# Kernel optimization log

Measured on AMD Instinct MI355X. Metric: run time of the kernel, lower is better.

The kernel has to match this reference:

```python
import jax, jax.numpy as jnp
import numpy as np

J = 24  # fixed pooling window (SampleLength/N = 1200/50)


def setup_inputs() -> dict:
    key = jax.random.key(0)
    k1, k2, k3 = jax.random.split(key, 3)
    T, N, K, C = 786432, 50, 400, 10  # T = 32768 segments * J
    x = jax.random.normal(k1, (T, N), dtype=jnp.float32)
    W1 = jax.random.normal(k2, (K, N), dtype=jnp.float32) * 0.1
    W2 = jax.random.normal(k3, (C, K), dtype=jnp.float32) * 0.1
    return {"x": x, "W1": W1, "W2": W2}


def reference(x, W1, W2):
    # linear + relu: [T, N] @ [N, K] -> [T, K]
    local_features = jax.nn.relu(jnp.einsum('tn,kn->tk', x, W1))
    # fixed-window mean over consecutive J rows: [T, K] -> [T//J, K]
    T, K = local_features.shape
    features = local_features.reshape(T // J, J, K).mean(axis=1)
    # final linear: [T//J, K] @ [K, C] -> [T//J, C]
    logits = jnp.einsum('bk,ck->bc', features, W2)
    return logits
```

## Files before the change

### kernel.cpp

```cpp
#include <hip/hip_runtime.h>
#include <hip/hip_bf16.h>

#define T_TOTAL 786432
#define N_IN 50
#define K_FEAT 400
#define C_OUT 10
#define ROWS_PER_CHUNK 48
#define NCHUNKS (T_TOTAL / ROWS_PER_CHUNK)
#define CPB 4
#define NBLOCKS (NCHUNKS / CPB)
#define NTHREADS 320
#define XS_STRIDE 72
#define XS_ROWS (CPB * ROWS_PER_CHUNK)

#define W1F_TASKS (25 * 2 * 64)
#define W2T_OFF_BYTES 51200
#define W2T_FLOATS (25 * NTHREADS)
#define PREP_TASKS (W1F_TASKS + W2T_FLOATS)

typedef __bf16 bfx8 __attribute__((ext_vector_type(8)));
typedef short  s16x8 __attribute__((ext_vector_type(8)));
typedef float  f32x4 __attribute__((ext_vector_type(4)));

static __device__ __forceinline__ short f2bf(float f) {
    union { float f; unsigned u; } v; v.f = f;
    unsigned r = v.u + 0x7fffu + ((v.u >> 16) & 1u);
    return (short)(r >> 16);
}

__global__ void prep_kernel(const float* __restrict__ W1,
                            const float* __restrict__ W2,
                            short* __restrict__ w1f, float* __restrict__ w2t)
{
    const int gid = blockIdx.x * blockDim.x + threadIdx.x;
    if (gid < W1F_TASKS) {
        const int lane = gid & 63;
        const int s    = (gid >> 6) & 1;
        const int tile = gid >> 7;
        const int m16  = lane & 15;
        const int quad = lane >> 4;
        const float* row = W1 + (tile * 16 + m16) * N_IN;
        s16x8 v;
        #pragma unroll
        for (int j = 0; j < 8; ++j) {
            const int n = s * 32 + quad * 8 + j;
            v[j] = (n < N_IN) ? f2bf(row[n]) : (short)0;
        }
        *(s16x8*)&w1f[gid * 8] = v;
    } else if (gid < PREP_TASKS) {
        const int i   = gid - W1F_TASKS;
        const int j   = i / NTHREADS;
        const int tid = i - j * NTHREADS;
        const int o    = tid >> 4;
        const int part = tid & 15;
        const int seg  = (o >= 10) ? 1 : 0;
        const int cls  = o - seg * 10;
        w2t[i] = W2[cls * K_FEAT + part * 25 + j];
    }
}

__global__ __launch_bounds__(NTHREADS) void classifier_kernel(
    const float* __restrict__ x, const short* __restrict__ w1f,
    const float* __restrict__ w2t, float* __restrict__ out)
{
    __shared__ short xs[XS_ROWS * XS_STRIDE];
    __shared__ float pooled[2 * K_FEAT];

    const int tid  = threadIdx.x;
    const int wave = tid >> 6;
    const int lane = tid & 63;
    const int m16  = lane & 15;
    const int quad = lane >> 4;

    {
        const float* xb = x + (size_t)blockIdx.x * (XS_ROWS * N_IN);
        #pragma unroll
        for (int it = 0; it < (XS_ROWS * 25) / NTHREADS; ++it) {
            const int i = tid + it * NTHREADS;
            const int r = i / 25;
            const int c2 = i - r * 25;
            const float2 v = *(const float2*)(xb + 2 * i);
            const int packed = (unsigned short)f2bf(v.x) |
                               ((unsigned)(unsigned short)f2bf(v.y) << 16);
            *(int*)&xs[r * XS_STRIDE + 2 * c2] = packed;
        }
        for (int i = tid; i < XS_ROWS * 7; i += NTHREADS) {
            const int r = i / 7;
            const int c = 50 + 2 * (i - r * 7);
            *(int*)&xs[r * XS_STRIDE + c] = 0;
        }
    }

    s16x8 bfrag[5][2];
    {
        const s16x8* wf = (const s16x8*)w1f;
        #pragma unroll
        for (int t = 0; t < 5; ++t) {
            #pragma unroll
            for (int s = 0; s < 2; ++s)
                bfrag[t][s] = wf[((wave * 5 + t) * 2 + s) * 64 + lane];
        }
    }

    const int o    = tid >> 4;
    const int part = tid & 15;
    const int segO = (o >= 10) ? 1 : 0;
    const int cls  = o - segO * 10;
    float w2r[25];
    #pragma unroll
    for (int j = 0; j < 25; ++j) w2r[j] = w2t[j * NTHREADS + tid];

    __syncthreads();

    for (int ciq = 0; ciq < CPB; ++ciq) {
        s16x8 a[3][2];
        #pragma unroll
        for (int r = 0; r < 3; ++r) {
            const short* arow =
                &xs[(ciq * ROWS_PER_CHUNK + r * 16 + m16) * XS_STRIDE + quad * 8];
            a[r][0] = *(const s16x8*)(arow);
            a[r][1] = *(const s16x8*)(arow + 32);
        }

        #pragma unroll
        for (int t = 0; t < 5; ++t) {
            float c0 = 0.f, c1 = 0.f;
            #pragma unroll
            for (int r = 0; r < 3; ++r) {
                f32x4 acc = {0.f, 0.f, 0.f, 0.f};
                acc = __builtin_amdgcn_mfma_f32_16x16x32_bf16(
                        __builtin_bit_cast(bfx8, a[r][0]),
                        __builtin_bit_cast(bfx8, bfrag[t][0]), acc, 0, 0, 0);
                acc = __builtin_amdgcn_mfma_f32_16x16x32_bf16(
                        __builtin_bit_cast(bfx8, a[r][1]),
                        __builtin_bit_cast(bfx8, bfrag[t][1]), acc, 0, 0, 0);
                const float s = fmaxf(acc[0], 0.f) + fmaxf(acc[1], 0.f)
                              + fmaxf(acc[2], 0.f) + fmaxf(acc[3], 0.f);
                const int g = r * 4 + quad;
                if (g < 6) c0 += s; else c1 += s;
            }
            c0 += __shfl_xor(c0, 16);
            c0 += __shfl_xor(c0, 32);
            c1 += __shfl_xor(c1, 16);
            c1 += __shfl_xor(c1, 32);
            if (quad == 0) {
                const int feat = (wave * 5 + t) * 16 + m16;
                pooled[feat] = c0;
                pooled[K_FEAT + feat] = c1;
            }
        }
        __syncthreads();

        float sum = 0.f;
        const float* pv = &pooled[segO * K_FEAT + part * 25];
        #pragma unroll
        for (int j = 0; j < 25; ++j) sum += pv[j] * w2r[j];
        sum += __shfl_down(sum, 8, 16);
        sum += __shfl_down(sum, 4, 16);
        sum += __shfl_down(sum, 2, 16);
        sum += __shfl_down(sum, 1, 16);
        if (part == 0) {
            const int chunk = blockIdx.x * CPB + ciq;
            out[(chunk * 2 + segO) * C_OUT + cls] = sum * (1.0f / 24.0f);
        }
        __syncthreads();
    }
}

extern "C" void kernel_launch(void* const* d_in, const int* in_sizes, int n_in,
                              void* d_out, int out_size, void* d_ws, size_t ws_size,
                              hipStream_t stream) {
    const float* x  = (const float*)d_in[0];
    const float* W1 = (const float*)d_in[1];
    const float* W2 = (const float*)d_in[2];
    float* out = (float*)d_out;

    short* w1f = (short*)d_ws;
    float* w2t = (float*)((char*)d_ws + W2T_OFF_BYTES);

    prep_kernel<<<(PREP_TASKS + 255) / 256, 256, 0, stream>>>(W1, W2, w1f, w2t);
    classifier_kernel<<<NBLOCKS, NTHREADS, 0, stream>>>(x, w1f, w2t, out);
}
```

Before: 288.0 us.

## Split into register-resident phase1 pooling kernel and MFMA phase2 classifier via workspace

Replaces the single LDS-staged kernel with two kernels. Phase 1 has each wave load x rows straight into registers as bf16 MFMA fragments and stream all 25 W1 tiles with a prefetch, writing pooled features as bf16 to a workspace buffer. Phase 2 runs the final 400->10 projection as MFMA over the pooled rows. The aim is to drop the LDS staging and block-level syncs and to raise occupancy. In exchange it adds a global round-trip of pooled features, loses precision by rounding them to bf16, and adds an extra launch. The old kernel is kept as a fallback when the workspace is too small.

```diff
diff --git a/kernel.cpp b/kernel.cpp
--- a/kernel.cpp
+++ b/kernel.cpp
@@ -5,18 +5,17 @@
 #define N_IN 50
 #define K_FEAT 400
 #define C_OUT 10
-#define ROWS_PER_CHUNK 48
-#define NCHUNKS (T_TOTAL / ROWS_PER_CHUNK)
-#define CPB 4
-#define NBLOCKS (NCHUNKS / CPB)
-#define NTHREADS 320
-#define XS_STRIDE 72
-#define XS_ROWS (CPB * ROWS_PER_CHUNK)
+#define NSEG 32768
 
 #define W1F_TASKS (25 * 2 * 64)
 #define W2T_OFF_BYTES 51200
-#define W2T_FLOATS (25 * NTHREADS)
-#define PREP_TASKS (W1F_TASKS + W2T_FLOATS)
+#define W2T_FLOATS (25 * 320)
+#define W2F_OFF_BYTES 83200
+#define W2F_TASKS (13 * 64)
+#define PREP_TASKS (W1F_TASKS + W2T_FLOATS + W2F_TASKS)
+#define POOLED_OFF_BYTES 98304
+#define POOLED_STRIDE 416
+#define WS_NEEDED (POOLED_OFF_BYTES + (size_t)NSEG * POOLED_STRIDE * 2)
 
 typedef __bf16 bfx8 __attribute__((ext_vector_type(8)));
 typedef short  s16x8 __attribute__((ext_vector_type(8)));
@@ -30,7 +29,8 @@
 
 __global__ void prep_kernel(const float* __restrict__ W1,
                             const float* __restrict__ W2,
-                            short* __restrict__ w1f, float* __restrict__ w2t)
+                            short* __restrict__ w1f, float* __restrict__ w2t,
+                            short* __restrict__ w2f)
 {
     const int gid = blockIdx.x * blockDim.x + threadIdx.x;
     if (gid < W1F_TASKS) {
@@ -47,47 +47,181 @@
             v[j] = (n < N_IN) ? f2bf(row[n]) : (short)0;
         }
         *(s16x8*)&w1f[gid * 8] = v;
-    } else if (gid < PREP_TASKS) {
+    } else if (gid < W1F_TASKS + W2T_FLOATS) {
         const int i   = gid - W1F_TASKS;
-        const int j   = i / NTHREADS;
-        const int tid = i - j * NTHREADS;
+        const int j   = i / 320;
+        const int tid = i - j * 320;
         const int o    = tid >> 4;
         const int part = tid & 15;
         const int seg  = (o >= 10) ? 1 : 0;
         const int cls  = o - seg * 10;
         w2t[i] = W2[cls * K_FEAT + part * 25 + j];
-    }
-}
-
-__global__ __launch_bounds__(NTHREADS) void classifier_kernel(
+    } else if (gid < PREP_TASKS) {
+        const int i    = gid - W1F_TASKS - W2T_FLOATS;
+        const int lane = i & 63;
+        const int kt   = i >> 6;
+        const int m16  = lane & 15;
+        const int quad = lane >> 4;
+        s16x8 v;
+        #pragma unroll
+        for (int j = 0; j < 8; ++j) {
+            const int feat = kt * 32 + quad * 8 + j;
+            v[j] = (m16 < C_OUT && feat < K_FEAT) ? f2bf(W2[m16 * K_FEAT + feat])
+                                                  : (short)0;
+        }
+        *(s16x8*)&w2f[i * 8] = v;
+    }
+}
+
+__global__ __launch_bounds__(256, 3) void phase1_kernel(
     const float* __restrict__ x, const short* __restrict__ w1f,
-    const float* __restrict__ w2t, float* __restrict__ out)
+    short* __restrict__ pooled)
 {
-    __shared__ short xs[XS_ROWS * XS_STRIDE];
-    __shared__ float pooled[2 * K_FEAT];
-
     const int tid  = threadIdx.x;
     const int wave = tid >> 6;
     const int lane = tid & 63;
     const int m16  = lane & 15;
     const int quad = lane >> 4;
+    const int wgid = blockIdx.x * 4 + wave;
+    const s16x8* wf = (const s16x8*)w1f;
+
+    for (int g = 0; g < 2; ++g) {
+        const int group = wgid * 2 + g;
+        const float* xg = x + (size_t)group * (2 * 48 * N_IN);
+
+        s16x8 A[6][2];
+        #pragma unroll
+        for (int ct = 0; ct < 6; ++ct) {
+            const float* rp = xg + (ct * 16 + m16) * N_IN;
+            float v0[8], v1[8];
+            #pragma unroll
+            for (int h = 0; h < 4; ++h) {
+                const float2 u = *(const float2*)(rp + quad * 8 + 2 * h);
+                v0[2 * h] = u.x; v0[2 * h + 1] = u.y;
+            }
+            if (quad < 2) {
+                #pragma unroll
+                for (int h = 0; h < 4; ++h) {
+                    const float2 u = *(const float2*)(rp + 32 + quad * 8 + 2 * h);
+                    v1[2 * h] = u.x; v1[2 * h + 1] = u.y;
+                }
+            } else if (quad == 2) {
+                const float2 u = *(const float2*)(rp + 48);
+                v1[0] = u.x; v1[1] = u.y;
+                #pragma unroll
+                for (int j = 2; j < 8; ++j) v1[j] = 0.f;
+            } else {
+                #pragma unroll
+                for (int j = 0; j < 8; ++j) v1[j] = 0.f;
+            }
+            s16x8 f0, f1;
+            #pragma unroll
+            for (int j = 0; j < 8; ++j) { f0[j] = f2bf(v0[j]); f1[j] = f2bf(v1[j]); }
+            A[ct][0] = f0; A[ct][1] = f1;
+        }
+
+        s16x8 b0 = wf[lane];
+        s16x8 b1 = wf[64 + lane];
+        const int seg0 = group * 4;
+        for (int t = 0; t < 25; ++t) {
+            const int tn = (t < 24) ? t + 1 : 24;
+            const s16x8 nb0 = wf[(tn * 2) * 64 + lane];
+            const s16x8 nb1 = wf[(tn * 2 + 1) * 64 + lane];
+            #pragma unroll
+            for (int h = 0; h < 2; ++h) {
+                float c0 = 0.f, c1 = 0.f;
+                #pragma unroll
+                for (int r = 0; r < 3; ++r) {
+                    f32x4 acc = {0.f, 0.f, 0.f, 0.f};
+                    acc = __builtin_amdgcn_mfma_f32_16x16x32_bf16(
+                            __builtin_bit_cast(bfx8, A[h * 3 + r][0]),
+                            __builtin_bit_cast(bfx8, b0), acc, 0, 0, 0);
+                    acc = __builtin_amdgcn_mfma_f32_16x16x32_bf16(
+                            __builtin_bit_cast(bfx8, A[h * 3 + r][1]),
+                            __builtin_bit_cast(bfx8, b1), acc, 0, 0, 0);
+                    const float s = fmaxf(acc[0], 0.f) + fmaxf(acc[1], 0.f)
+                                  + fmaxf(acc[2], 0.f) + fmaxf(acc[3], 0.f);
+                    if (r * 4 + quad < 6) c0 += s; else c1 += s;
+                }
+                c0 += __shfl_xor(c0, 16); c0 += __shfl_xor(c0, 32);
+                c1 += __shfl_xor(c1, 16); c1 += __shfl_xor(c1, 32);
+                if (quad < 2) {
+                    const int seg = seg0 + 2 * h + quad;
+                    const float cv = (quad == 0) ? c0 : c1;
+                    pooled[(size_t)seg * POOLED_STRIDE + t * 16 + m16] = f2bf(cv);
+                }
+            }
+            b0 = nb0; b1 = nb1;
+        }
+    }
+}
+
+__global__ __launch_bounds__(256) void phase2_kernel(
+    const short* __restrict__ pooled, const short* __restrict__ w2f,
+    float* __restrict__ out)
+{
+    const int tid  = threadIdx.x;
+    const int lane = tid & 63;
+    const int m16  = lane & 15;
+    const int quad = lane >> 4;
+    const int segbase = (blockIdx.x * 4 + (tid >> 6)) * 16;
+    const s16x8* wf = (const s16x8*)w2f;
+    const short* arow = pooled + (size_t)(segbase + m16) * POOLED_STRIDE;
+
+    f32x4 acc = {0.f, 0.f, 0.f, 0.f};
+    s16x8 zero = {0, 0, 0, 0, 0, 0, 0, 0};
+    #pragma unroll
+    for (int kt = 0; kt < 13; ++kt) {
+        const s16x8 b = wf[kt * 64 + lane];
+        const s16x8 a = (kt == 12 && quad >= 2)
+                            ? zero
+                            : *(const s16x8*)(arow + kt * 32 + quad * 8);
+        acc = __builtin_amdgcn_mfma_f32_16x16x32_bf16(
+                __builtin_bit_cast(bfx8, a), __builtin_bit_cast(bfx8, b),
+                acc, 0, 0, 0);
+    }
+    if (m16 < C_OUT) {
+        #pragma unroll
+        for (int rg = 0; rg < 4; ++rg)
+            out[(size_t)(segbase + quad * 4 + rg) * C_OUT + m16] =
+                acc[rg] * (1.0f / 24.0f);
+    }
+}
+
+#define FB_CPB 4
+#define FB_NTHREADS 320
+#define FB_XS_STRIDE 72
+#define FB_XS_ROWS (FB_CPB * 48)
+
+__global__ __launch_bounds__(FB_NTHREADS) void classifier_fb(
+    const float* __restrict__ x, const short* __restrict__ w1f,
+    const float* __restrict__ w2t, float* __restrict__ out)
+{
+    __shared__ short xs[FB_XS_ROWS * FB_XS_STRIDE];
+    __shared__ float pooled[2 * K_FEAT];
+
+    const int tid  = threadIdx.x;
+    const int wave = tid >> 6;
+    const int lane = tid & 63;
+    const int m16  = lane & 15;
+    const int quad = lane >> 4;
 
     {
-        const float* xb = x + (size_t)blockIdx.x * (XS_ROWS * N_IN);
-        #pragma unroll
-        for (int it = 0; it < (XS_ROWS * 25) / NTHREADS; ++it) {
-            const int i = tid + it * NTHREADS;
+        const float* xb = x + (size_t)blockIdx.x * (FB_XS_ROWS * N_IN);
+        #pragma unroll
+        for (int it = 0; it < (FB_XS_ROWS * 25) / FB_NTHREADS; ++it) {
+            const int i = tid + it * FB_NTHREADS;
             const int r = i / 25;
             const int c2 = i - r * 25;
             const float2 v = *(const float2*)(xb + 2 * i);
             const int packed = (unsigned short)f2bf(v.x) |
                                ((unsigned)(unsigned short)f2bf(v.y) << 16);
-            *(int*)&xs[r * XS_STRIDE + 2 * c2] = packed;
-        }
-        for (int i = tid; i < XS_ROWS * 7; i += NTHREADS) {
+            *(int*)&xs[r * FB_XS_STRIDE + 2 * c2] = packed;
+        }
+        for (int i = tid; i < FB_XS_ROWS * 7; i += FB_NTHREADS) {
             const int r = i / 7;
             const int c = 50 + 2 * (i - r * 7);
-            *(int*)&xs[r * XS_STRIDE + c] = 0;
+            *(int*)&xs[r * FB_XS_STRIDE + c] = 0;
         }
     }
 
@@ -95,11 +229,10 @@
     {
         const s16x8* wf = (const s16x8*)w1f;
         #pragma unroll
-        for (int t = 0; t < 5; ++t) {
+        for (int t = 0; t < 5; ++t)
             #pragma unroll
             for (int s = 0; s < 2; ++s)
                 bfrag[t][s] = wf[((wave * 5 + t) * 2 + s) * 64 + lane];
-        }
     }
 
     const int o    = tid >> 4;
@@ -108,20 +241,19 @@
     const int cls  = o - segO * 10;
     float w2r[25];
     #pragma unroll
-    for (int j = 0; j < 25; ++j) w2r[j] = w2t[j * NTHREADS + tid];
+    for (int j = 0; j < 25; ++j) w2r[j] = w2t[j * FB_NTHREADS + tid];
 
     __syncthreads();
 
-    for (int ciq = 0; ciq < CPB; ++ciq) {
+    for (int ciq = 0; ciq < FB_CPB; ++ciq) {
         s16x8 a[3][2];
         #pragma unroll
         for (int r = 0; r < 3; ++r) {
             const short* arow =
-                &xs[(ciq * ROWS_PER_CHUNK + r * 16 + m16) * XS_STRIDE + quad * 8];
+                &xs[(ciq * 48 + r * 16 + m16) * FB_XS_STRIDE + quad * 8];
             a[r][0] = *(const s16x8*)(arow);
             a[r][1] = *(const s16x8*)(arow + 32);
         }
-
         #pragma unroll
         for (int t = 0; t < 5; ++t) {
             float c0 = 0.f, c1 = 0.f;
@@ -136,13 +268,10 @@
                         __builtin_bit_cast(bfx8, bfrag[t][1]), acc, 0, 0, 0);
                 const float s = fmaxf(acc[0], 0.f) + fmaxf(acc[1], 0.f)
                               + fmaxf(acc[2], 0.f) + fmaxf(acc[3], 0.f);
-                const int g = r * 4 + quad;
-                if (g < 6) c0 += s; else c1 += s;
-            }
-            c0 += __shfl_xor(c0, 16);
-            c0 += __shfl_xor(c0, 32);
-            c1 += __shfl_xor(c1, 16);
-            c1 += __shfl_xor(c1, 32);
+                if (r * 4 + quad < 6) c0 += s; else c1 += s;
+            }
+            c0 += __shfl_xor(c0, 16); c0 += __shfl_xor(c0, 32);
+            c1 += __shfl_xor(c1, 16); c1 += __shfl_xor(c1, 32);
             if (quad == 0) {
                 const int feat = (wave * 5 + t) * 16 + m16;
                 pooled[feat] = c0;
@@ -160,7 +289,7 @@
         sum += __shfl_down(sum, 2, 16);
         sum += __shfl_down(sum, 1, 16);
         if (part == 0) {
-            const int chunk = blockIdx.x * CPB + ciq;
+            const int chunk = blockIdx.x * FB_CPB + ciq;
             out[(chunk * 2 + segO) * C_OUT + cls] = sum * (1.0f / 24.0f);
         }
         __syncthreads();
@@ -177,7 +306,15 @@
 
     short* w1f = (short*)d_ws;
     float* w2t = (float*)((char*)d_ws + W2T_OFF_BYTES);
-
-    prep_kernel<<<(PREP_TASKS + 255) / 256, 256, 0, stream>>>(W1, W2, w1f, w2t);
-    classifier_kernel<<<NBLOCKS, NTHREADS, 0, stream>>>(x, w1f, w2t, out);
-}
+    short* w2f = (short*)((char*)d_ws + W2F_OFF_BYTES);
+    short* pooled = (short*)((char*)d_ws + POOLED_OFF_BYTES);
+
+    prep_kernel<<<(PREP_TASKS + 255) / 256, 256, 0, stream>>>(W1, W2, w1f, w2t, w2f);
+
+    if (ws_size >= WS_NEEDED) {
+        phase1_kernel<<<1024, 256, 0, stream>>>(x, w1f, pooled);
+        phase2_kernel<<<512, 256, 0, stream>>>(pooled, w2f, out);
+    } else {
+        classifier_fb<<<4096, FB_NTHREADS, 0, stream>>>(x, w1f, w2t, out);
+    }
+}
```

Result: no change. 289.5 us (+0.5%).
